# Performance work log

Measured on AMD Instinct MI355X. Metric: run time of the kernel, lower is better.

Reference implementation:

```python
import jax, jax.numpy as jnp
from jax import lax
import numpy as np

B, T, IN, H = 8192, 512, 5, 32


def setup_inputs() -> dict:
    key = jax.random.key(0)
    ks = jax.random.split(key, 7)
    s_ih = 1.0 / np.sqrt(H)
    return {
        "x": jax.random.normal(ks[0], (B, T, IN), dtype=jnp.float32),
        "W_ih": jax.random.normal(ks[1], (4 * H, IN), dtype=jnp.float32) * s_ih,
        "W_hh": jax.random.normal(ks[2], (4 * H, H), dtype=jnp.float32) * s_ih,
        "b_ih": jax.random.normal(ks[3], (4 * H,), dtype=jnp.float32) * s_ih,
        "b_hh": jax.random.normal(ks[4], (4 * H,), dtype=jnp.float32) * s_ih,
        "W_fc": jax.random.normal(ks[5], (1, H), dtype=jnp.float32) * s_ih,
        "b_fc": jax.random.normal(ks[6], (1,), dtype=jnp.float32) * s_ih,
    }


def reference(x, W_ih, W_hh, b_ih, b_hh, W_fc, b_fc):
    # x: [B, T, IN]. Single-layer batch-first LSTM (PyTorch gate order i,f,g,o),
    # then linear head on the final timestep's hidden state.
    b = x.shape[0]
    h0 = jnp.zeros((b, H), x.dtype)
    c0 = jnp.zeros((b, H), x.dtype)
    # Precompute input projections for all timesteps in one GEMM: [T, B, 4H]
    x_t = jnp.swapaxes(x, 0, 1)  # [T, B, IN]
    x_proj = jnp.einsum("tbi,gi->tbg", x_t, W_ih) + b_ih + b_hh

    def step(carry, xp):
        h, c = carry
        gates = xp + h @ W_hh.T  # [B, 4H]
        i, f, g, o = jnp.split(gates, 4, axis=-1)
        i = jax.nn.sigmoid(i)
        f = jax.nn.sigmoid(f)
        g = jnp.tanh(g)
        o = jax.nn.sigmoid(o)
        c = f * c + i * g
        h = o * jnp.tanh(c)
        return (h, c), None

    (h_last, _), _ = lax.scan(step, (h0, c0), x_proj)
    return h_last @ W_fc.T + b_fc  # [B, 1]
```

## Files before the change

### kernel.cpp

```cpp
#include <hip/hip_runtime.h>


typedef __attribute__((ext_vector_type(8))) short short8;
typedef __attribute__((ext_vector_type(4))) float f32x4;

static constexpr int BB  = 8192;
static constexpr int TT  = 512;
static constexpr int NIN = 5;
static constexpr int HH  = 32;

__device__ __forceinline__ unsigned short bf_rne(float f) {
    unsigned int u = __float_as_uint(f);
    u = (u + 0x7FFFu + ((u >> 16) & 1u)) >> 16;
    return (unsigned short)u;
}
__device__ __forceinline__ float bf_f32(unsigned short h) {
    return __uint_as_float((unsigned int)h << 16);
}
__device__ __forceinline__ float fast_sigmoid(float x) {
    float e = __builtin_amdgcn_exp2f(-1.4426950408889634f * x);
    return __builtin_amdgcn_rcpf(1.0f + e);
}
__device__ __forceinline__ float fast_tanh(float x) {
    float e = __builtin_amdgcn_exp2f(2.8853900817779268f * x);
    return 1.0f - 2.0f * __builtin_amdgcn_rcpf(1.0f + e);
}

__global__ __launch_bounds__(256, 2) void lstm_mfma(
    const float* __restrict__ x,
    const float* __restrict__ W_ih,
    const float* __restrict__ W_hh,
    const float* __restrict__ b_ih,
    const float* __restrict__ b_hh,
    const float* __restrict__ W_fc,
    const float* __restrict__ b_fc,
    float* __restrict__ out)
{
    const int tid  = threadIdx.x;
    const int lane = tid & 63;
    const int w    = tid >> 6;
    const int jh   = w >> 1;
    const int rh   = w & 1;
    const int col  = lane & 15;
    const int kg   = lane >> 4;
    const int b0   = blockIdx.x * 16;

    __shared__ __align__(16) unsigned char hb[2][16 * 128];
    __shared__ float parts[32];

    {
        unsigned int* p = (unsigned int*)&hb[0][0];
#pragma unroll
        for (int q = 0; q < 4; ++q) p[tid + q * 256] = 0u;
    }

    short8 bhi[4], blo[4], b1[4];
#pragma unroll
    for (int t4 = 0; t4 < 4; ++t4) {
        const int r = t4 * 32 + jh * 16 + col;
#pragma unroll
        for (int e = 0; e < 8; ++e) {
            float wv = W_hh[r * HH + kg * 8 + e];
            unsigned short hh = bf_rne(wv);
            bhi[t4][e] = (short)hh;
            blo[t4][e] = (short)bf_rne(wv - bf_f32(hh));
        }
        float bias = b_ih[r] + b_hh[r];
        unsigned short bh = bf_rne(bias);
        unsigned short bl = bf_rne(bias - bf_f32(bh));
        short8 v;
#pragma unroll
        for (int e = 0; e < 8; ++e) v[e] = 0;
        if (kg == 0 || kg == 1) {
#pragma unroll
            for (int e = 0; e < NIN; ++e) v[e] = (short)bf_rne(W_ih[r * NIN + e]);
            v[5] = (short)((kg == 0) ? bh : bl);
        } else if (kg == 2) {
#pragma unroll
            for (int e = 0; e < NIN; ++e) {
                float wv = W_ih[r * NIN + e];
                unsigned short h2 = bf_rne(wv);
                v[e] = (short)bf_rne(wv - bf_f32(h2));
            }
        }
        b1[t4] = v;
    }

    __syncthreads();

    const float* xb = x + (size_t)(b0 + col) * (TT * NIN);
    float xc[NIN];
#pragma unroll
    for (int e = 0; e < NIN; ++e) xc[e] = xb[e];

    float c0 = 0.f, c1 = 0.f, h0f = 0.f, h1f = 0.f;

#pragma unroll 2
    for (int t = 0; t < TT; ++t) {
        const int cur = t & 1, nxt = cur ^ 1;

        const int tn = (t + 1 < TT) ? (t + 1) : t;
        float xn[NIN];
#pragma unroll
        for (int e = 0; e < NIN; ++e) xn[e] = xb[tn * NIN + e];

        const unsigned int ro = ((unsigned)(kg * 16)) ^ (((unsigned)(col & 7)) << 4);
        short8 a0 = *(const short8*)&hb[cur][col * 128 + ro];

        unsigned short xh[NIN], xl[NIN];
#pragma unroll
        for (int e = 0; e < NIN; ++e) {
            unsigned short h = bf_rne(xc[e]);
            xh[e] = h;
            xl[e] = bf_rne(xc[e] - bf_f32(h));
        }
        short8 a1;
#pragma unroll
        for (int e = 0; e < NIN; ++e) {
            unsigned short s = (kg == 1) ? xl[e] : xh[e];
            a1[e] = (kg == 3) ? (short)0 : (short)s;
        }
        a1[5] = (kg < 2) ? (short)0x3F80 : (short)0;
        a1[6] = 0; a1[7] = 0;

        const f32x4 z = {0.f, 0.f, 0.f, 0.f};
        f32x4 ai = __builtin_amdgcn_mfma_f32_16x16x32_bf16(a0, blo[0], z, 0, 0, 0);
        ai = __builtin_amdgcn_mfma_f32_16x16x32_bf16(a0, bhi[0], ai, 0, 0, 0);
        ai = __builtin_amdgcn_mfma_f32_16x16x32_bf16(a1, b1[0],  ai, 0, 0, 0);
        f32x4 af = __builtin_amdgcn_mfma_f32_16x16x32_bf16(a0, blo[1], z, 0, 0, 0);
        af = __builtin_amdgcn_mfma_f32_16x16x32_bf16(a0, bhi[1], af, 0, 0, 0);
        af = __builtin_amdgcn_mfma_f32_16x16x32_bf16(a1, b1[1],  af, 0, 0, 0);
        f32x4 ag = __builtin_amdgcn_mfma_f32_16x16x32_bf16(a0, blo[2], z, 0, 0, 0);
        ag = __builtin_amdgcn_mfma_f32_16x16x32_bf16(a0, bhi[2], ag, 0, 0, 0);
        ag = __builtin_amdgcn_mfma_f32_16x16x32_bf16(a1, b1[2],  ag, 0, 0, 0);
        f32x4 ao = __builtin_amdgcn_mfma_f32_16x16x32_bf16(a0, blo[3], z, 0, 0, 0);
        ao = __builtin_amdgcn_mfma_f32_16x16x32_bf16(a0, bhi[3], ao, 0, 0, 0);
        ao = __builtin_amdgcn_mfma_f32_16x16x32_bf16(a1, b1[3],  ao, 0, 0, 0);

        const int j = jh * 16 + col;
        {
            float iv = fast_sigmoid(rh ? ai[2] : ai[0]);
            float fv = fast_sigmoid(rh ? af[2] : af[0]);
            float gv = fast_tanh   (rh ? ag[2] : ag[0]);
            float ov = fast_sigmoid(rh ? ao[2] : ao[0]);
            c0 = fv * c0 + iv * gv;
            h0f = ov * fast_tanh(c0);
            const int m = kg * 4 + rh * 2 + 0;
            const unsigned int off = ((unsigned)(j * 2)) ^ (((unsigned)(m & 7)) << 4);
            *(unsigned short*)&hb[nxt][m * 128 + off] = bf_rne(h0f);
        }
        {
            float iv = fast_sigmoid(rh ? ai[3] : ai[1]);
            float fv = fast_sigmoid(rh ? af[3] : af[1]);
            float gv = fast_tanh   (rh ? ag[3] : ag[1]);
            float ov = fast_sigmoid(rh ? ao[3] : ao[1]);
            c1 = fv * c1 + iv * gv;
            h1f = ov * fast_tanh(c1);
            const int m = kg * 4 + rh * 2 + 1;
            const unsigned int off = ((unsigned)(j * 2)) ^ (((unsigned)(m & 7)) << 4);
            *(unsigned short*)&hb[nxt][m * 128 + off] = bf_rne(h1f);
        }

#pragma unroll
        for (int e = 0; e < NIN; ++e) xc[e] = xn[e];

        __syncthreads();
    }

    const int j = jh * 16 + col;
    const float wfc = W_fc[j];
    float v0 = h0f * wfc, v1 = h1f * wfc;
    v0 += __shfl_xor(v0, 1); v0 += __shfl_xor(v0, 2);
    v0 += __shfl_xor(v0, 4); v0 += __shfl_xor(v0, 8);
    v1 += __shfl_xor(v1, 1); v1 += __shfl_xor(v1, 2);
    v1 += __shfl_xor(v1, 4); v1 += __shfl_xor(v1, 8);
    if (col == 0) {
        parts[jh * 16 + kg * 4 + rh * 2 + 0] = v0;
        parts[jh * 16 + kg * 4 + rh * 2 + 1] = v1;
    }
    __syncthreads();
    if (tid < 16) out[b0 + tid] = parts[tid] + parts[16 + tid] + b_fc[0];
}

extern "C" void kernel_launch(void* const* d_in, const int* in_sizes, int n_in,
                              void* d_out, int out_size, void* d_ws, size_t ws_size,
                              hipStream_t stream) {
    const float* x    = (const float*)d_in[0];
    const float* W_ih = (const float*)d_in[1];
    const float* W_hh = (const float*)d_in[2];
    const float* b_ih = (const float*)d_in[3];
    const float* b_hh = (const float*)d_in[4];
    const float* W_fc = (const float*)d_in[5];
    const float* b_fc = (const float*)d_in[6];
    float* out = (float*)d_out;

    lstm_mfma<<<dim3(BB / 16), dim3(256), 0, stream>>>(
        x, W_ih, W_hh, b_ih, b_hh, W_fc, b_fc, out);
}
```

Before: 335.0 us.

## Use 8 waves per block and prepack x into bf16 hi/lo pairs

Doubles the block to 512 threads, so each wave handles one row of the MFMA output instead of two. This halves the per-wave gate and activation work on the serial critical path. A separate pre-pass kernel splits x into bf16 hi/lo pairs in workspace, which removes the per-step conversion in the recurrent loop but adds a large global write and read (128 MB) on a different path. It also replaces __syncthreads with an explicit lgkmcnt wait plus s_barrier, and moves the final head reduction into shared memory.

New measurement: 503.1 us. 50.2% more time.

```diff
diff --git a/kernel.cpp b/kernel.cpp
--- a/kernel.cpp
+++ b/kernel.cpp
@@ -3,6 +3,7 @@
 
 typedef __attribute__((ext_vector_type(8))) short short8;
 typedef __attribute__((ext_vector_type(4))) float f32x4;
+typedef __attribute__((ext_vector_type(4))) unsigned int u32x4;
 
 static constexpr int BB  = 8192;
 static constexpr int TT  = 512;
@@ -26,8 +27,28 @@
     return 1.0f - 2.0f * __builtin_amdgcn_rcpf(1.0f + e);
 }
 
-__global__ __launch_bounds__(256, 2) void lstm_mfma(
+__global__ __launch_bounds__(256) void pack_x(const float* __restrict__ x,
+                                              unsigned int* __restrict__ xp) {
+    int idx = blockIdx.x * 256 + threadIdx.x;
+    if (idx >= BB * TT) return;
+    const float* s = x + (size_t)idx * NIN;
+    unsigned int w[NIN];
+#pragma unroll
+    for (int e = 0; e < NIN; ++e) {
+        float v = s[e];
+        unsigned short hi = bf_rne(v);
+        unsigned short lo = bf_rne(v - bf_f32(hi));
+        w[e] = (unsigned int)hi | ((unsigned int)lo << 16);
+    }
+    unsigned int* d = xp + (size_t)idx * 8;
+    *(u32x4*)d = (u32x4){w[0], w[1], w[2], w[3]};
+    d[4] = w[4];
+}
+
+template <bool PACKED>
+__global__ __launch_bounds__(512, 4) void lstm_mfma8(
     const float* __restrict__ x,
+    const unsigned int* __restrict__ xpk,
     const float* __restrict__ W_ih,
     const float* __restrict__ W_hh,
     const float* __restrict__ b_ih,
@@ -39,19 +60,18 @@
     const int tid  = threadIdx.x;
     const int lane = tid & 63;
     const int w    = tid >> 6;
-    const int jh   = w >> 1;
-    const int rh   = w & 1;
+    const int jh   = w & 1;
+    const int rq   = w >> 1;
     const int col  = lane & 15;
     const int kg   = lane >> 4;
     const int b0   = blockIdx.x * 16;
 
-    __shared__ __align__(16) unsigned char hb[2][16 * 128];
-    __shared__ float parts[32];
+    __shared__ __align__(16) unsigned char hb[2][2048];
 
     {
-        unsigned int* p = (unsigned int*)&hb[0][0];
-#pragma unroll
-        for (int q = 0; q < 4; ++q) p[tid + q * 256] = 0u;
+        unsigned int* p = (unsigned int*)hb;
+        p[tid] = 0u;
+        p[tid + 512] = 0u;
     }
 
     short8 bhi[4], blo[4], b1[4];
@@ -88,42 +108,75 @@
 
     __syncthreads();
 
-    const float* xb = x + (size_t)(b0 + col) * (TT * NIN);
-    float xc[NIN];
-#pragma unroll
-    for (int e = 0; e < NIN; ++e) xc[e] = xb[e];
-
-    float c0 = 0.f, c1 = 0.f, h0f = 0.f, h1f = 0.f;
-
-#pragma unroll 2
-    for (int t = 0; t < TT; ++t) {
-        const int cur = t & 1, nxt = cur ^ 1;
+    const unsigned shiftv = (kg == 1) ? 16u : 0u;
+    const unsigned maskv  = (kg == 3) ? 0u : 0xFFFFu;
+    const unsigned b5hi   = (kg < 2) ? (0x3F80u << 16) : 0u;
+
+    const int m = kg * 4 + rq;
+    const int j = jh * 16 + col;
+    const unsigned wroff = (unsigned)(m * 128) + (((unsigned)(j * 2)) ^ (((unsigned)(m & 7)) << 4));
+    const unsigned rdoff = (unsigned)(col * 128) + (((unsigned)(kg * 16)) ^ (((unsigned)(col & 7)) << 4));
+
+    const int bcol = b0 + col;
+    const unsigned int* xq = xpk + (size_t)bcol * TT * 8;
+    const float* xf = x + (size_t)bcol * (TT * NIN);
+
+    unsigned int wx[NIN];
+    float xsc[NIN];
+    if (PACKED) {
+        u32x4 q = *(const u32x4*)xq;
+        wx[0] = q[0]; wx[1] = q[1]; wx[2] = q[2]; wx[3] = q[3]; wx[4] = xq[4];
+    } else {
+#pragma unroll
+        for (int e = 0; e < NIN; ++e) xsc[e] = xf[e];
+    }
+
+    float c = 0.f, hreg = 0.f;
+    const f32x4 z = {0.f, 0.f, 0.f, 0.f};
+
+    auto step = [&](int t, int cur) {
+        const int nxt = cur ^ 1;
 
         const int tn = (t + 1 < TT) ? (t + 1) : t;
-        float xn[NIN];
-#pragma unroll
-        for (int e = 0; e < NIN; ++e) xn[e] = xb[tn * NIN + e];
-
-        const unsigned int ro = ((unsigned)(kg * 16)) ^ (((unsigned)(col & 7)) << 4);
-        short8 a0 = *(const short8*)&hb[cur][col * 128 + ro];
-
-        unsigned short xh[NIN], xl[NIN];
-#pragma unroll
-        for (int e = 0; e < NIN; ++e) {
-            unsigned short h = bf_rne(xc[e]);
-            xh[e] = h;
-            xl[e] = bf_rne(xc[e] - bf_f32(h));
-        }
+        unsigned int nwx[NIN];
+        float nxs[NIN];
+        if (PACKED) {
+            const unsigned int* p = xq + (size_t)tn * 8;
+            u32x4 q = *(const u32x4*)p;
+            nwx[0] = q[0]; nwx[1] = q[1]; nwx[2] = q[2]; nwx[3] = q[3]; nwx[4] = p[4];
+        } else {
+#pragma unroll
+            for (int e = 0; e < NIN; ++e) nxs[e] = xf[tn * NIN + e];
+        }
+
+        short8 a0 = *(const short8*)&hb[cur][rdoff];
+
         short8 a1;
-#pragma unroll
-        for (int e = 0; e < NIN; ++e) {
-            unsigned short s = (kg == 1) ? xl[e] : xh[e];
-            a1[e] = (kg == 3) ? (short)0 : (short)s;
-        }
-        a1[5] = (kg < 2) ? (short)0x3F80 : (short)0;
-        a1[6] = 0; a1[7] = 0;
-
-        const f32x4 z = {0.f, 0.f, 0.f, 0.f};
+        if (PACKED) {
+            unsigned h0 = (wx[0] >> shiftv) & maskv;
+            unsigned h1 = (wx[1] >> shiftv) & maskv;
+            unsigned h2 = (wx[2] >> shiftv) & maskv;
+            unsigned h3 = (wx[3] >> shiftv) & maskv;
+            unsigned h4 = (wx[4] >> shiftv) & maskv;
+            u32x4 uu = {h0 | (h1 << 16), h2 | (h3 << 16), h4 | b5hi, 0u};
+            a1 = __builtin_bit_cast(short8, uu);
+        } else {
+            unsigned short xh[NIN], xl[NIN];
+#pragma unroll
+            for (int e = 0; e < NIN; ++e) {
+                unsigned short h = bf_rne(xsc[e]);
+                xh[e] = h;
+                xl[e] = bf_rne(xsc[e] - bf_f32(h));
+            }
+#pragma unroll
+            for (int e = 0; e < NIN; ++e) {
+                unsigned short s = (kg == 1) ? xl[e] : xh[e];
+                a1[e] = (kg == 3) ? (short)0 : (short)s;
+            }
+            a1[5] = (kg < 2) ? (short)0x3F80 : (short)0;
+            a1[6] = 0; a1[7] = 0;
+        }
+
         f32x4 ai = __builtin_amdgcn_mfma_f32_16x16x32_bf16(a0, blo[0], z, 0, 0, 0);
         ai = __builtin_amdgcn_mfma_f32_16x16x32_bf16(a0, bhi[0], ai, 0, 0, 0);
         ai = __builtin_amdgcn_mfma_f32_16x16x32_bf16(a1, b1[0],  ai, 0, 0, 0);
@@ -137,49 +190,48 @@
         ao = __builtin_amdgcn_mfma_f32_16x16x32_bf16(a0, bhi[3], ao, 0, 0, 0);
         ao = __builtin_amdgcn_mfma_f32_16x16x32_bf16(a1, b1[3],  ao, 0, 0, 0);
 
-        const int j = jh * 16 + col;
-        {
-            float iv = fast_sigmoid(rh ? ai[2] : ai[0]);
-            float fv = fast_sigmoid(rh ? af[2] : af[0]);
-            float gv = fast_tanh   (rh ? ag[2] : ag[0]);
-            float ov = fast_sigmoid(rh ? ao[2] : ao[0]);
-            c0 = fv * c0 + iv * gv;
-            h0f = ov * fast_tanh(c0);
-            const int m = kg * 4 + rh * 2 + 0;
-            const unsigned int off = ((unsigned)(j * 2)) ^ (((unsigned)(m & 7)) << 4);
-            *(unsigned short*)&hb[nxt][m * 128 + off] = bf_rne(h0f);
-        }
-        {
-            float iv = fast_sigmoid(rh ? ai[3] : ai[1]);
-            float fv = fast_sigmoid(rh ? af[3] : af[1]);
-            float gv = fast_tanh   (rh ? ag[3] : ag[1]);
-            float ov = fast_sigmoid(rh ? ao[3] : ao[1]);
-            c1 = fv * c1 + iv * gv;
-            h1f = ov * fast_tanh(c1);
-            const int m = kg * 4 + rh * 2 + 1;
-            const unsigned int off = ((unsigned)(j * 2)) ^ (((unsigned)(m & 7)) << 4);
-            *(unsigned short*)&hb[nxt][m * 128 + off] = bf_rne(h1f);
-        }
-
-#pragma unroll
-        for (int e = 0; e < NIN; ++e) xc[e] = xn[e];
-
-        __syncthreads();
-    }
-
-    const int j = jh * 16 + col;
-    const float wfc = W_fc[j];
-    float v0 = h0f * wfc, v1 = h1f * wfc;
-    v0 += __shfl_xor(v0, 1); v0 += __shfl_xor(v0, 2);
-    v0 += __shfl_xor(v0, 4); v0 += __shfl_xor(v0, 8);
-    v1 += __shfl_xor(v1, 1); v1 += __shfl_xor(v1, 2);
-    v1 += __shfl_xor(v1, 4); v1 += __shfl_xor(v1, 8);
-    if (col == 0) {
-        parts[jh * 16 + kg * 4 + rh * 2 + 0] = v0;
-        parts[jh * 16 + kg * 4 + rh * 2 + 1] = v1;
-    }
+        float gi, gf, gg, go;
+        switch (rq) {
+            case 0:  gi = ai[0]; gf = af[0]; gg = ag[0]; go = ao[0]; break;
+            case 1:  gi = ai[1]; gf = af[1]; gg = ag[1]; go = ao[1]; break;
+            case 2:  gi = ai[2]; gf = af[2]; gg = ag[2]; go = ao[2]; break;
+            default: gi = ai[3]; gf = af[3]; gg = ag[3]; go = ao[3]; break;
+        }
+        float iv = fast_sigmoid(gi);
+        float fv = fast_sigmoid(gf);
+        float gv = fast_tanh(gg);
+        float ov = fast_sigmoid(go);
+        c = fv * c + iv * gv;
+        hreg = ov * fast_tanh(c);
+        *(unsigned short*)&hb[nxt][wroff] = bf_rne(hreg);
+
+        if (PACKED) {
+#pragma unroll
+            for (int e = 0; e < NIN; ++e) wx[e] = nwx[e];
+        } else {
+#pragma unroll
+            for (int e = 0; e < NIN; ++e) xsc[e] = nxs[e];
+        }
+
+        asm volatile("s_waitcnt lgkmcnt(0)" ::: "memory");
+        __builtin_amdgcn_s_barrier();
+    };
+
+#pragma unroll 1
+    for (int t = 0; t < TT; t += 2) {
+        step(t, 0);
+        step(t + 1, 1);
+    }
+
+    float* sc = (float*)hb;
+    sc[m * 32 + j] = hreg * W_fc[j];
     __syncthreads();
-    if (tid < 16) out[b0 + tid] = parts[tid] + parts[16 + tid] + b_fc[0];
+    if (tid < 16) {
+        float s = b_fc[0];
+#pragma unroll
+        for (int q = 0; q < HH; ++q) s += sc[tid * 32 + q];
+        out[b0 + tid] = s;
+    }
 }
 
 extern "C" void kernel_launch(void* const* d_in, const int* in_sizes, int n_in,
@@ -194,6 +246,14 @@
     const float* b_fc = (const float*)d_in[6];
     float* out = (float*)d_out;
 
-    lstm_mfma<<<dim3(BB / 16), dim3(256), 0, stream>>>(
-        x, W_ih, W_hh, b_ih, b_hh, W_fc, b_fc, out);
-}
+    const size_t need = (size_t)BB * TT * 8 * sizeof(unsigned int);
+    if (ws_size >= need) {
+        unsigned int* xp = (unsigned int*)d_ws;
+        pack_x<<<dim3((BB * TT + 255) / 256), dim3(256), 0, stream>>>(x, xp);
+        lstm_mfma8<true><<<dim3(BB / 16), dim3(512), 0, stream>>>(
+            x, xp, W_ih, W_hh, b_ih, b_hh, W_fc, b_fc, out);
+    } else {
+        lstm_mfma8<false><<<dim3(BB / 16), dim3(512), 0, stream>>>(
+            x, nullptr, W_ih, W_hh, b_ih, b_hh, W_fc, b_fc, out);
+    }
+}
```

## Run each LSTM batch tile in a single wavefront with shuffle-based hidden exchange

Applied to the files above, without the earlier changes.

Each block is now one 64-lane wave that handles 8 batch rows, down from 256 threads handling 16. The roles of the MFMA operands are swapped so the weights sit in A registers (8 gate tiles) and h is the B operand. The hidden state is redistributed with cross-lane shuffles instead of LDS double buffering plus __syncthreads, and x is loaded once per lane then broadcast by shuffle. This removes the per-timestep block barrier and LDS round trip, at the cost of twice the MFMA count per batch row (half the B columns are wasted) and more per-lane register pressure.

Result: no change. 330.2 us (-1.4%).

```diff
diff --git a/kernel.cpp b/kernel.cpp
--- a/kernel.cpp
+++ b/kernel.cpp
@@ -3,6 +3,7 @@
 
 typedef __attribute__((ext_vector_type(8))) short short8;
 typedef __attribute__((ext_vector_type(4))) float f32x4;
+typedef __attribute__((ext_vector_type(4))) unsigned int u32x4;
 
 static constexpr int BB  = 8192;
 static constexpr int TT  = 512;
@@ -26,7 +27,7 @@
     return 1.0f - 2.0f * __builtin_amdgcn_rcpf(1.0f + e);
 }
 
-__global__ __launch_bounds__(256, 2) void lstm_mfma(
+__global__ __launch_bounds__(64) void lstm_wave(
     const float* __restrict__ x,
     const float* __restrict__ W_ih,
     const float* __restrict__ W_hh,
@@ -36,150 +37,142 @@
     const float* __restrict__ b_fc,
     float* __restrict__ out)
 {
-    const int tid  = threadIdx.x;
-    const int lane = tid & 63;
-    const int w    = tid >> 6;
-    const int jh   = w >> 1;
-    const int rh   = w & 1;
+    const int lane = threadIdx.x & 63;
     const int col  = lane & 15;
     const int kg   = lane >> 4;
-    const int b0   = blockIdx.x * 16;
+    const int b0   = blockIdx.x * 8;
+    const int bloc = col & 7;
+    const bool jlow = (col < 8);
+    const int jbase = 4 * kg + (jlow ? 0 : 16);
 
-    __shared__ __align__(16) unsigned char hb[2][16 * 128];
-    __shared__ float parts[32];
-
-    {
-        unsigned int* p = (unsigned int*)&hb[0][0];
+    short8 Ahh_hi[8], Ahh_lo[8], Ax[8];
 #pragma unroll
-        for (int q = 0; q < 4; ++q) p[tid + q * 256] = 0u;
-    }
-
-    short8 bhi[4], blo[4], b1[4];
-#pragma unroll
-    for (int t4 = 0; t4 < 4; ++t4) {
-        const int r = t4 * 32 + jh * 16 + col;
+    for (int t4 = 0; t4 < 8; ++t4) {
+        const int gr = 16 * t4 + col;
 #pragma unroll
         for (int e = 0; e < 8; ++e) {
-            float wv = W_hh[r * HH + kg * 8 + e];
-            unsigned short hh = bf_rne(wv);
-            bhi[t4][e] = (short)hh;
-            blo[t4][e] = (short)bf_rne(wv - bf_f32(hh));
+            float wv = W_hh[gr * HH + kg * 8 + e];
+            unsigned short hi = bf_rne(wv);
+            Ahh_hi[t4][e] = (short)hi;
+            Ahh_lo[t4][e] = (short)bf_rne(wv - bf_f32(hi));
         }
-        float bias = b_ih[r] + b_hh[r];
-        unsigned short bh = bf_rne(bias);
-        unsigned short bl = bf_rne(bias - bf_f32(bh));
+        float bias = b_ih[gr] + b_hh[gr];
+        unsigned short bh_ = bf_rne(bias);
+        unsigned short bl_ = bf_rne(bias - bf_f32(bh_));
         short8 v;
 #pragma unroll
         for (int e = 0; e < 8; ++e) v[e] = 0;
         if (kg == 0 || kg == 1) {
 #pragma unroll
-            for (int e = 0; e < NIN; ++e) v[e] = (short)bf_rne(W_ih[r * NIN + e]);
-            v[5] = (short)((kg == 0) ? bh : bl);
+            for (int e = 0; e < NIN; ++e) v[e] = (short)bf_rne(W_ih[gr * NIN + e]);
+            v[5] = (short)((kg == 0) ? bh_ : bl_);
         } else if (kg == 2) {
 #pragma unroll
             for (int e = 0; e < NIN; ++e) {
-                float wv = W_ih[r * NIN + e];
+                float wv = W_ih[gr * NIN + e];
                 unsigned short h2 = bf_rne(wv);
                 v[e] = (short)bf_rne(wv - bf_f32(h2));
             }
         }
-        b1[t4] = v;
+        Ax[t4] = v;
     }
 
-    __syncthreads();
+    const int xb = (lane / 5 < 8) ? (lane / 5) : 7;
+    int xe = lane - 5 * xb; if (xe > 4) xe = 4;
+    const float* px = x + ((size_t)(b0 + xb) * TT) * NIN + xe;
 
-    const float* xb = x + (size_t)(b0 + col) * (TT * NIN);
-    float xc[NIN];
+    const unsigned shx  = (kg == 1) ? 16u : 0u;
+    const unsigned mskx = (kg == 3) ? 0u : 0xFFFFu;
+    const unsigned one5 = (kg < 2) ? (0x3F80u << 16) : 0u;
+
+    const int srcA = 32 * (kg & 1) + bloc + 8 * (kg >> 1);
+    const int srcB = srcA + 16;
+
+    float xv = px[0]; px += NIN;
+    unsigned int xpk = 0;
+    {
+        unsigned short hi = bf_rne(xv);
+        unsigned short lo = bf_rne(xv - bf_f32(hi));
+        xpk = (unsigned int)hi | ((unsigned int)lo << 16);
+    }
+
+    unsigned int bh0 = 0, bh1 = 0, bh2 = 0, bh3 = 0;
+    float c0 = 0.f, c1 = 0.f, c2 = 0.f, c3 = 0.f;
+    float h0 = 0.f, h1 = 0.f, h2 = 0.f, h3 = 0.f;
+
+    const f32x4 z = {0.f, 0.f, 0.f, 0.f};
+
+#pragma unroll 1
+    for (int t = 0; t < TT; ++t) {
+        float xvn = xv;
+        if (t + 1 < TT) { xvn = px[0]; px += NIN; }
+
+        unsigned int p0x = (unsigned)__shfl((int)xpk, 5 * bloc + 0, 64);
+        unsigned int p1x = (unsigned)__shfl((int)xpk, 5 * bloc + 1, 64);
+        unsigned int p2x = (unsigned)__shfl((int)xpk, 5 * bloc + 2, 64);
+        unsigned int p3x = (unsigned)__shfl((int)xpk, 5 * bloc + 3, 64);
+        unsigned int p4x = (unsigned)__shfl((int)xpk, 5 * bloc + 4, 64);
+        unsigned int a0 = (p0x >> shx) & mskx;
+        unsigned int a1 = (p1x >> shx) & mskx;
+        unsigned int a2 = (p2x >> shx) & mskx;
+        unsigned int a3 = (p3x >> shx) & mskx;
+        unsigned int a4 = (p4x >> shx) & mskx;
+        u32x4 bxu = {a0 | (a1 << 16), a2 | (a3 << 16), a4 | one5, 0u};
+        short8 bx = __builtin_bit_cast(short8, bxu);
+        u32x4 bhu = {bh0, bh1, bh2, bh3};
+        short8 bh = __builtin_bit_cast(short8, bhu);
+
+        f32x4 acc[8];
 #pragma unroll
-    for (int e = 0; e < NIN; ++e) xc[e] = xb[e];
+        for (int t4 = 0; t4 < 8; ++t4)
+            acc[t4] = __builtin_amdgcn_mfma_f32_16x16x32_bf16(Ahh_lo[t4], bh, z, 0, 0, 0);
+#pragma unroll
+        for (int t4 = 0; t4 < 8; ++t4)
+            acc[t4] = __builtin_amdgcn_mfma_f32_16x16x32_bf16(Ahh_hi[t4], bh, acc[t4], 0, 0, 0);
+#pragma unroll
+        for (int t4 = 0; t4 < 8; ++t4)
+            acc[t4] = __builtin_amdgcn_mfma_f32_16x16x32_bf16(Ax[t4], bx, acc[t4], 0, 0, 0);
 
-    float c0 = 0.f, c1 = 0.f, h0f = 0.f, h1f = 0.f;
-
-#pragma unroll 2
-    for (int t = 0; t < TT; ++t) {
-        const int cur = t & 1, nxt = cur ^ 1;
-
-        const int tn = (t + 1 < TT) ? (t + 1) : t;
-        float xn[NIN];
 #pragma unroll
-        for (int e = 0; e < NIN; ++e) xn[e] = xb[tn * NIN + e];
-
-        const unsigned int ro = ((unsigned)(kg * 16)) ^ (((unsigned)(col & 7)) << 4);
-        short8 a0 = *(const short8*)&hb[cur][col * 128 + ro];
-
-        unsigned short xh[NIN], xl[NIN];
-#pragma unroll
-        for (int e = 0; e < NIN; ++e) {
-            unsigned short h = bf_rne(xc[e]);
-            xh[e] = h;
-            xl[e] = bf_rne(xc[e] - bf_f32(h));
-        }
-        short8 a1;
-#pragma unroll
-        for (int e = 0; e < NIN; ++e) {
-            unsigned short s = (kg == 1) ? xl[e] : xh[e];
-            a1[e] = (kg == 3) ? (short)0 : (short)s;
-        }
-        a1[5] = (kg < 2) ? (short)0x3F80 : (short)0;
-        a1[6] = 0; a1[7] = 0;
-
-        const f32x4 z = {0.f, 0.f, 0.f, 0.f};
-        f32x4 ai = __builtin_amdgcn_mfma_f32_16x16x32_bf16(a0, blo[0], z, 0, 0, 0);
-        ai = __builtin_amdgcn_mfma_f32_16x16x32_bf16(a0, bhi[0], ai, 0, 0, 0);
-        ai = __builtin_amdgcn_mfma_f32_16x16x32_bf16(a1, b1[0],  ai, 0, 0, 0);
-        f32x4 af = __builtin_amdgcn_mfma_f32_16x16x32_bf16(a0, blo[1], z, 0, 0, 0);
-        af = __builtin_amdgcn_mfma_f32_16x16x32_bf16(a0, bhi[1], af, 0, 0, 0);
-        af = __builtin_amdgcn_mfma_f32_16x16x32_bf16(a1, b1[1],  af, 0, 0, 0);
-        f32x4 ag = __builtin_amdgcn_mfma_f32_16x16x32_bf16(a0, blo[2], z, 0, 0, 0);
-        ag = __builtin_amdgcn_mfma_f32_16x16x32_bf16(a0, bhi[2], ag, 0, 0, 0);
-        ag = __builtin_amdgcn_mfma_f32_16x16x32_bf16(a1, b1[2],  ag, 0, 0, 0);
-        f32x4 ao = __builtin_amdgcn_mfma_f32_16x16x32_bf16(a0, blo[3], z, 0, 0, 0);
-        ao = __builtin_amdgcn_mfma_f32_16x16x32_bf16(a0, bhi[3], ao, 0, 0, 0);
-        ao = __builtin_amdgcn_mfma_f32_16x16x32_bf16(a1, b1[3],  ao, 0, 0, 0);
-
-        const int j = jh * 16 + col;
-        {
-            float iv = fast_sigmoid(rh ? ai[2] : ai[0]);
-            float fv = fast_sigmoid(rh ? af[2] : af[0]);
-            float gv = fast_tanh   (rh ? ag[2] : ag[0]);
-            float ov = fast_sigmoid(rh ? ao[2] : ao[0]);
-            c0 = fv * c0 + iv * gv;
-            h0f = ov * fast_tanh(c0);
-            const int m = kg * 4 + rh * 2 + 0;
-            const unsigned int off = ((unsigned)(j * 2)) ^ (((unsigned)(m & 7)) << 4);
-            *(unsigned short*)&hb[nxt][m * 128 + off] = bf_rne(h0f);
-        }
-        {
-            float iv = fast_sigmoid(rh ? ai[3] : ai[1]);
-            float fv = fast_sigmoid(rh ? af[3] : af[1]);
-            float gv = fast_tanh   (rh ? ag[3] : ag[1]);
-            float ov = fast_sigmoid(rh ? ao[3] : ao[1]);
-            c1 = fv * c1 + iv * gv;
-            h1f = ov * fast_tanh(c1);
-            const int m = kg * 4 + rh * 2 + 1;
-            const unsigned int off = ((unsigned)(j * 2)) ^ (((unsigned)(m & 7)) << 4);
-            *(unsigned short*)&hb[nxt][m * 128 + off] = bf_rne(h1f);
+        for (int r = 0; r < 4; ++r) {
+            float gi = jlow ? acc[0][r] : acc[1][r];
+            float gf = jlow ? acc[2][r] : acc[3][r];
+            float gg = jlow ? acc[4][r] : acc[5][r];
+            float go = jlow ? acc[6][r] : acc[7][r];
+            float iv = fast_sigmoid(gi);
+            float fv = fast_sigmoid(gf);
+            float gv = fast_tanh(gg);
+            float ov = fast_sigmoid(go);
+            float cc = (r == 0 ? c0 : r == 1 ? c1 : r == 2 ? c2 : c3);
+            cc = fv * cc + iv * gv;
+            float hh = ov * fast_tanh(cc);
+            if (r == 0) { c0 = cc; h0 = hh; }
+            else if (r == 1) { c1 = cc; h1 = hh; }
+            else if (r == 2) { c2 = cc; h2 = hh; }
+            else { c3 = cc; h3 = hh; }
         }
 
-#pragma unroll
-        for (int e = 0; e < NIN; ++e) xc[e] = xn[e];
+        unsigned int p0 = (unsigned int)bf_rne(h0) | ((unsigned int)bf_rne(h1) << 16);
+        unsigned int p1 = (unsigned int)bf_rne(h2) | ((unsigned int)bf_rne(h3) << 16);
+        bh0 = (unsigned)__shfl((int)p0, srcA, 64);
+        bh1 = (unsigned)__shfl((int)p1, srcA, 64);
+        bh2 = (unsigned)__shfl((int)p0, srcB, 64);
+        bh3 = (unsigned)__shfl((int)p1, srcB, 64);
 
-        __syncthreads();
+        {
+            unsigned short hi = bf_rne(xvn);
+            unsigned short lo = bf_rne(xvn - bf_f32(hi));
+            xpk = (unsigned int)hi | ((unsigned int)lo << 16);
+        }
+        xv = xvn;
     }
 
-    const int j = jh * 16 + col;
-    const float wfc = W_fc[j];
-    float v0 = h0f * wfc, v1 = h1f * wfc;
-    v0 += __shfl_xor(v0, 1); v0 += __shfl_xor(v0, 2);
-    v0 += __shfl_xor(v0, 4); v0 += __shfl_xor(v0, 8);
-    v1 += __shfl_xor(v1, 1); v1 += __shfl_xor(v1, 2);
-    v1 += __shfl_xor(v1, 4); v1 += __shfl_xor(v1, 8);
-    if (col == 0) {
-        parts[jh * 16 + kg * 4 + rh * 2 + 0] = v0;
-        parts[jh * 16 + kg * 4 + rh * 2 + 1] = v1;
-    }
-    __syncthreads();
-    if (tid < 16) out[b0 + tid] = parts[tid] + parts[16 + tid] + b_fc[0];
+    float v = h0 * W_fc[jbase + 0] + h1 * W_fc[jbase + 1]
+            + h2 * W_fc[jbase + 2] + h3 * W_fc[jbase + 3];
+    v += __shfl_xor(v, 8);
+    v += __shfl_xor(v, 16);
+    v += __shfl_xor(v, 32);
+    if (lane < 8) out[b0 + lane] = v + b_fc[0];
 }
 
 extern "C" void kernel_launch(void* const* d_in, const int* in_sizes, int n_in,
@@ -194,6 +187,6 @@
     const float* b_fc = (const float*)d_in[6];
     float* out = (float*)d_out;
 
-    lstm_mfma<<<dim3(BB / 16), dim3(256), 0, stream>>>(
+    lstm_wave<<<dim3(BB / 8), dim3(64), 0, stream>>>(
         x, W_ih, W_hh, b_ih, b_hh, W_fc, b_fc, out);
 }
```
